# Optimization experiments

Hardware: AMD Instinct MI355X
Metric: run time of the kernel (lower is better)

## Reference

```python
import jax, jax.numpy as jnp
import numpy as np

BN_EPS = 1e-5


def setup_inputs() -> dict:
    key = jax.random.key(0)
    ks = jax.random.split(key, 12)
    B, C, N = 8, 256, 2048
    s = 1.0 / np.sqrt(C)
    x = jax.random.normal(ks[0], (B, C, N), dtype=jnp.float32)
    gamma = jnp.ones((C,), jnp.float32)
    beta = jnp.zeros((C,), jnp.float32)
    Wq = jax.random.normal(ks[1], (C, C), jnp.float32) * s
    bq = jnp.zeros((C,), jnp.float32)
    Wk = jax.random.normal(ks[2], (C, C), jnp.float32) * s
    bk = jnp.zeros((C,), jnp.float32)
    Wv = jax.random.normal(ks[3], (C, C), jnp.float32) * s
    bv = jnp.zeros((C,), jnp.float32)
    Wp = jax.random.normal(ks[4], (C, C), jnp.float32) * s
    bp = jnp.zeros((C,), jnp.float32)
    return {"x": x, "gamma": gamma, "beta": beta, "Wq": Wq, "bq": bq,
            "Wk": Wk, "bk": bk, "Wv": Wv, "bv": bv, "Wp": Wp, "bp": bp}


def reference(x, gamma, beta, Wq, bq, Wk, bk, Wv, bv, Wp, bp):
    B, C, N = x.shape
    # BatchNorm1d (training-mode batch stats): normalize per channel over (B, N)
    mean = jnp.mean(x, axis=(0, 2), keepdims=True)            # [1,C,1]
    var = jnp.mean(jnp.square(x - mean), axis=(0, 2), keepdims=True)
    h = (x - mean) * jax.lax.rsqrt(var + BN_EPS)
    h = h * gamma[None, :, None] + beta[None, :, None]
    # 1x1 Conv1d projections == per-position channel GEMMs
    q = jnp.einsum('oc,bcn->bno', Wq, h) + bq[None, None, :]  # [B,N,C]
    k = jnp.einsum('oc,bcn->bon', Wk, h) + bk[None, :, None]  # [B,C,N]
    v = jnp.einsum('oc,bcn->bno', Wv, h) + bv[None, None, :]  # [B,N,C]
    scale = jnp.asarray(C, x.dtype) ** -0.5
    w = jnp.einsum('bnc,bcm->bnm', q, k) * scale              # [B,N,N]
    w = jax.nn.softmax(w, axis=-1)
    h = jnp.einsum('bnm,bmc->bnc', w, v)                      # [B,N,C]
    out = jnp.einsum('oc,bnc->bon', Wp, h) + bp[None, :, None]  # [B,C,N]
    return x + out
```

## Files before the change

### kernel.cpp

```cpp
#include <hip/hip_runtime.h>
#include <hip/hip_fp16.h>

typedef _Float16 f16x8 __attribute__((ext_vector_type(8)));
typedef _Float16 f16x4 __attribute__((ext_vector_type(4)));
typedef float f32x4 __attribute__((ext_vector_type(4)));
typedef float f32x16 __attribute__((ext_vector_type(16)));

#define MFMA16(a, b, c) __builtin_amdgcn_mfma_f32_16x16x32_f16(a, b, c, 0, 0, 0)
#define MFMA32(a, b, c) __builtin_amdgcn_mfma_f32_32x32x16_f16(a, b, c, 0, 0, 0)

__device__ __forceinline__ void gload_lds16(const _Float16* g, void* l) {
    __builtin_amdgcn_global_load_lds(
        (const __attribute__((address_space(1))) void*)g,
        (__attribute__((address_space(3))) void*)l, 16, 0, 0);
}

__device__ __forceinline__ unsigned pkh(float a, float b) {
    typedef __fp16 fp16v2 __attribute__((ext_vector_type(2)));
    fp16v2 h = __builtin_amdgcn_cvt_pkrtz(a, b);
    return __builtin_bit_cast(unsigned, h);
}

__device__ __forceinline__ float fexp2(float x) {
#if __has_builtin(__builtin_amdgcn_exp2f)
    return __builtin_amdgcn_exp2f(x);
#else
    return exp2f(x);
#endif
}

__global__ __launch_bounds__(256) void trans_stats_kernel(
    const float* __restrict__ x, _Float16* __restrict__ xt,
    float* __restrict__ sums)
{
    __shared__ float tile[64][65];
    int t = threadIdx.x;
    int b = blockIdx.z, c0 = blockIdx.y * 64, n0 = blockIdx.x * 64;
    int nl = t & 63, cq = t >> 6;
#pragma unroll
    for (int r = 0; r < 16; ++r) {
        int cl = cq * 16 + r;
        tile[cl][nl] = x[((size_t)b * 256 + c0 + cl) * 2048 + n0 + nl];
    }
    __syncthreads();
    int cl2 = t & 63, nq = t >> 6;
#pragma unroll
    for (int r = 0; r < 16; ++r) {
        int nl2 = nq * 16 + r;
        xt[((size_t)b * 2048 + n0 + nl2) * 256 + c0 + cl2] = (_Float16)tile[cl2][nl2];
    }
    if (t < 64) {
        float s = 0.f, ss = 0.f;
#pragma unroll
        for (int j = 0; j < 64; ++j) {
            float v = tile[t][j];
            s += v; ss += v * v;
        }
        atomicAdd(&sums[c0 + t], s);
        atomicAdd(&sums[256 + c0 + t], ss);
    }
}

__global__ __launch_bounds__(256) void fold_kernel(
    const float* __restrict__ Wq, const float* __restrict__ Wk,
    const float* __restrict__ Wv, const float* __restrict__ Wp,
    const float* __restrict__ bq, const float* __restrict__ bk,
    const float* __restrict__ bv,
    const float* __restrict__ gamma, const float* __restrict__ beta,
    const float* __restrict__ sums,
    _Float16* __restrict__ wbf, float* __restrict__ bfold)
{
    int t = threadIdx.x, bid = blockIdx.x;
    if (bid >= 192) {
        int i = (bid - 192) * 256 + t;
        wbf[3 * 65536 + i] = (_Float16)Wp[i];
        return;
    }
    __shared__ float sc[256], sh[256];
    if (t < 256) {
        float mean = sums[t] * (1.f / 16384.f);
        float var  = sums[256 + t] * (1.f / 16384.f) - mean * mean;
        float rstd = rsqrtf(var + 1e-5f);
        float s = rstd * gamma[t];
        sc[t] = s;
        sh[t] = beta[t] - mean * s;
    }
    __syncthreads();
    const float QS = 0.09016844005556021f;
    int mat = bid >> 6;
    int o = (bid & 63) * 4 + (t >> 6);
    int lane = t & 63;
    const float* W  = (mat == 0) ? Wq : (mat == 1) ? Wk : Wv;
    const float* bb = (mat == 0) ? bq : (mat == 1) ? bk : bv;
    float qs = (mat == 0) ? QS : 1.f;
    float dot = 0.f;
    _Float16* wd = wbf + mat * 65536 + o * 256;
#pragma unroll
    for (int i = 0; i < 4; ++i) {
        int c = lane * 4 + i;
        float wv_ = W[o * 256 + c];
        dot += wv_ * sh[c];
        wd[c] = (_Float16)(wv_ * sc[c] * qs);
    }
#pragma unroll
    for (int off = 32; off > 0; off >>= 1) dot += __shfl_down(dot, off, 64);
    if (lane == 0) bfold[mat * 256 + o] = qs * (bb[o] + dot);
}

template<int BN, int WGM, int WGN, typename OT, bool BIAS_I, bool RES, int EPI>
__global__ __launch_bounds__(256, 3) void gemm_nt(
    const _Float16* __restrict__ Aall, long strideA,
    const _Float16* __restrict__ Ball, long strideB,
    const float* __restrict__ bias,
    const float* __restrict__ resid, long strideR,
    OT* __restrict__ Call, long strideC, int Nn)
{
    constexpr int BM = 128;
    constexpr int WR = BM / WGM;
    constexpr int WC = BN / WGN;
    constexpr int FM = WR / 16, FN = WC / 16;
    constexpr int BUFSZ = 8192 + BN * 64;
    constexpr int NI = 8 + BN / 16;
    constexpr int PW = NI / 4;

    int b = blockIdx.z;
    const _Float16* A  = Aall + (size_t)b * strideA;
    const _Float16* Bm = Ball + (size_t)b * strideB;
    OT* C = Call + (size_t)b * strideC;
    int i0 = blockIdx.y * BM, j0 = blockIdx.x * BN;

    __shared__ __align__(16) char lds[2 * BUFSZ];

    int t = threadIdx.x, lane = t & 63, w = t >> 6;
    int lr = lane & 15, lg = lane >> 4;
    int wm = w % WGM, wn = w / WGM;

    int soff = (lane >> 2) * 256 + (((lane & 3) ^ ((lane >> 3) & 3))) * 8;
    int lgx16 = ((lg ^ ((lr >> 1) & 3))) * 16;

    f32x4 acc[FM][FN] = {};

    auto stage = [&](int kk, int buf) {
#pragma unroll
        for (int i = 0; i < PW; ++i) {
            int u = w * PW + i;
            if (u < 8)
                gload_lds16(A + (size_t)(i0 + u * 16) * 256 + kk * 32 + soff,
                            lds + buf * BUFSZ + u * 1024);
            else
                gload_lds16(Bm + (size_t)(j0 + (u - 8) * 16) * 256 + kk * 32 + soff,
                            lds + buf * BUFSZ + 8192 + (u - 8) * 1024);
        }
    };

    stage(0, 0);
    __syncthreads();
    int buf = 0;
#pragma unroll
    for (int kk = 0; kk < 8; ++kk) {
        if (kk + 1 < 8) stage(kk + 1, buf ^ 1);
        const char* ab = lds + buf * BUFSZ;
        const char* bb = ab + 8192;
        f16x8 af[FM], bf[FN];
#pragma unroll
        for (int f = 0; f < FM; ++f)
            af[f] = *(const f16x8*)(ab + (wm * WR + f * 16 + lr) * 64 + lgx16);
#pragma unroll
        for (int f = 0; f < FN; ++f)
            bf[f] = *(const f16x8*)(bb + (wn * WC + f * 16 + lr) * 64 + lgx16);
        __builtin_amdgcn_s_setprio(1);
#pragma unroll
        for (int fm = 0; fm < FM; ++fm)
#pragma unroll
            for (int fn = 0; fn < FN; ++fn)
                acc[fm][fn] = MFMA16(af[fm], bf[fn], acc[fm][fn]);
        __builtin_amdgcn_s_setprio(0);
        __syncthreads();
        buf ^= 1;
    }
    if constexpr (EPI == 0) {
#pragma unroll
        for (int fm = 0; fm < FM; ++fm)
#pragma unroll
            for (int fn = 0; fn < FN; ++fn)
#pragma unroll
                for (int rr = 0; rr < 4; ++rr) {
                    int row = i0 + wm * WR + fm * 16 + lg * 4 + rr;
                    int col = j0 + wn * WC + fn * 16 + lr;
                    float vv = acc[fm][fn][rr] + (BIAS_I ? bias[row] : bias[col]);
                    if (RES) vv += resid[(size_t)b * strideR + (size_t)row * Nn + col];
                    C[(size_t)row * Nn + col] = (OT)vv;
                }
    } else {
#pragma unroll
        for (int fm = 0; fm < FM; ++fm)
#pragma unroll
            for (int fn = 0; fn < FN; ++fn) {
                int row0 = i0 + wm * WR + fm * 16 + lg * 4;
                int col  = j0 + wn * WC + fn * 16 + lr;
                f16x4 q4;
#pragma unroll
                for (int rr = 0; rr < 4; ++rr) {
                    float vv = acc[fm][fn][rr] + (BIAS_I ? bias[row0 + rr] : bias[col]);
                    q4[rr] = (_Float16)vv;
                }
                size_t off;
                if constexpr (EPI == 1) {
                    int mt = col >> 5, mloc = col & 31;
                    int ks = row0 >> 4;
                    int ln2 = mloc + 32 * (lg >> 1);
                    off = (((size_t)mt * 16 + ks) * 64 + ln2) * 8 + (lg & 1) * 4;
                } else {
                    int mt = row0 >> 5, ms = (row0 >> 4) & 1;
                    int dt = col >> 5, dloc = col & 31;
                    int ln2 = dloc + 32 * (lg >> 1);
                    off = ((((size_t)mt * 2 + ms) * 8 + dt) * 64 + ln2) * 8 + (lg & 1) * 4;
                }
                *(f16x4*)((_Float16*)C + off) = q4;
            }
    }
}

__global__ __launch_bounds__(256, 2) void attn8_kernel(
    const _Float16* __restrict__ qb, const _Float16* __restrict__ kfrag,
    const _Float16* __restrict__ vfrag,
    _Float16* __restrict__ Opart, float* __restrict__ lpart,
    int nsp, int mspan)
{
    int id = blockIdx.x;
    int b = id & 7;
    int rest = id >> 3;
    int qblk = rest & 15, sp = rest >> 4;
    int T = mspan >> 5;

    __shared__ __align__(16) char lds[66560];

    int t = threadIdx.x, ln = t & 63, w = t >> 6;
    int col = ln & 31, hi = ln >> 5;

    const _Float16* kg = kfrag + (size_t)b * 524288 + (size_t)(sp * T) * 8192 + ln * 8;
    const _Float16* vg = vfrag + (size_t)b * 524288 + (size_t)(sp * T) * 8192 + ln * 8;
    int c0 = w * 4;
    int frd = ln * 16;

    f16x8 qf[16];
    {
        const _Float16* qp = qb + ((size_t)b * 2048 + qblk * 128 + w * 32 + col) * 256 + hi * 8;
#pragma unroll
        for (int ks = 0; ks < 16; ++ks) qf[ks] = *(const f16x8*)(qp + ks * 16);
    }

    f32x16 oacc[8] = {};
    float l_run = 0.f;
    unsigned W[8];

#pragma unroll
    for (int i = 0; i < 4; ++i) {
        int c = c0 + i;
        gload_lds16(kg + c * 512,        lds + c * 1024);
        gload_lds16(vg + c * 512,        lds + 16384 + c * 1024);
        gload_lds16(kg + 8192 + c * 512, lds + 32768 + c * 1024);
        gload_lds16(vg + 8192 + c * 512, lds + 49152 + c * 1024);
    }
    asm volatile("s_waitcnt vmcnt(0)" ::: "memory");
    __builtin_amdgcn_sched_barrier(0);
    __builtin_amdgcn_s_barrier();
    {
        f32x16 sn = {};
        __builtin_amdgcn_s_setprio(1);
#pragma unroll
        for (int ks = 0; ks < 16; ++ks) {
            f16x8 kf = *(const f16x8*)(lds + ks * 1024 + frd);
            sn = MFMA32(kf, qf[ks], sn);
        }
        __builtin_amdgcn_s_setprio(0);
        float pv_[16];
#pragma unroll
        for (int i = 0; i < 16; ++i) pv_[i] = fexp2(sn[i] - 16.f);
        float psum = ((pv_[0]+pv_[1]) + (pv_[2]+pv_[3])) + ((pv_[4]+pv_[5]) + (pv_[6]+pv_[7]))
                   + ((pv_[8]+pv_[9]) + (pv_[10]+pv_[11])) + ((pv_[12]+pv_[13]) + (pv_[14]+pv_[15]));
        psum += __shfl_xor(psum, 32, 64);
        l_run = psum;
        W[0] = pkh(pv_[0],  pv_[1]);  W[1] = pkh(pv_[2],  pv_[3]);
        W[2] = pkh(pv_[4],  pv_[5]);  W[3] = pkh(pv_[6],  pv_[7]);
        W[4] = pkh(pv_[8],  pv_[9]);  W[5] = pkh(pv_[10], pv_[11]);
        W[6] = pkh(pv_[12], pv_[13]); W[7] = pkh(pv_[14], pv_[15]);
    }
    __builtin_amdgcn_s_barrier();

    for (int tt = 0; tt < T - 1; ++tt) {
        char* myb = lds + (tt & 1) * 32768;
        char* nxb = lds + ((tt + 1) & 1) * 32768;
        if (tt + 2 < T) {
            const _Float16* ks2 = kg + (size_t)(tt + 2) * 8192;
#pragma unroll
            for (int i = 0; i < 4; ++i)
                gload_lds16(ks2 + (c0 + i) * 512, myb + (c0 + i) * 1024);
        }
        union { unsigned u[4]; f16x8 v; } pf0, pf1;
        {
            unsigned sx0 = hi ? W[0] : W[2], sx1 = hi ? W[1] : W[3];
            unsigned r0 = __shfl_xor(sx0, 32, 64), r1 = __shfl_xor(sx1, 32, 64);
            pf0.u[0] = hi ? r0 : W[0]; pf0.u[1] = hi ? r1 : W[1];
            pf0.u[2] = hi ? W[2] : r0; pf0.u[3] = hi ? W[3] : r1;
        }
        {
            unsigned sx0 = hi ? W[4] : W[6], sx1 = hi ? W[5] : W[7];
            unsigned r0 = __shfl_xor(sx0, 32, 64), r1 = __shfl_xor(sx1, 32, 64);
            pf1.u[0] = hi ? r0 : W[4]; pf1.u[1] = hi ? r1 : W[5];
            pf1.u[2] = hi ? W[6] : r0; pf1.u[3] = hi ? W[7] : r1;
        }
        f32x16 sn = {};
        __builtin_amdgcn_s_setprio(1);
#pragma unroll
        for (int g = 0; g < 4; ++g) {
#pragma unroll
            for (int k2 = 0; k2 < 4; ++k2) {
                int ks = g * 4 + k2;
                f16x8 kf = *(const f16x8*)(nxb + ks * 1024 + frd);
                sn = MFMA32(kf, qf[ks], sn);
            }
#pragma unroll
            for (int k2 = 0; k2 < 4; ++k2) {
                int idx = g * 4 + k2;
                f16x8 vf = *(const f16x8*)(myb + 16384 + idx * 1024 + frd);
                oacc[idx & 7] = MFMA32(vf, (g < 2) ? pf0.v : pf1.v, oacc[idx & 7]);
            }
        }
        __builtin_amdgcn_s_setprio(0);
        {
            float pv_[16];
#pragma unroll
            for (int i = 0; i < 16; ++i) pv_[i] = fexp2(sn[i] - 16.f);
            float psum = ((pv_[0]+pv_[1]) + (pv_[2]+pv_[3])) + ((pv_[4]+pv_[5]) + (pv_[6]+pv_[7]))
                       + ((pv_[8]+pv_[9]) + (pv_[10]+pv_[11])) + ((pv_[12]+pv_[13]) + (pv_[14]+pv_[15]));
            psum += __shfl_xor(psum, 32, 64);
            l_run += psum;
            W[0] = pkh(pv_[0],  pv_[1]);  W[1] = pkh(pv_[2],  pv_[3]);
            W[2] = pkh(pv_[4],  pv_[5]);  W[3] = pkh(pv_[6],  pv_[7]);
            W[4] = pkh(pv_[8],  pv_[9]);  W[5] = pkh(pv_[10], pv_[11]);
            W[6] = pkh(pv_[12], pv_[13]); W[7] = pkh(pv_[14], pv_[15]);
        }
        __builtin_amdgcn_s_barrier();
        __builtin_amdgcn_sched_barrier(0);
        if (tt + 2 < T) {
            const _Float16* vs2 = vg + (size_t)(tt + 2) * 8192;
#pragma unroll
            for (int i = 0; i < 4; ++i)
                gload_lds16(vs2 + (c0 + i) * 512, myb + 16384 + (c0 + i) * 1024);
        }
        asm volatile("s_waitcnt vmcnt(4)" ::: "memory");
        __builtin_amdgcn_sched_barrier(0);
        __builtin_amdgcn_s_barrier();
    }

    asm volatile("s_waitcnt vmcnt(0)" ::: "memory");
    __builtin_amdgcn_sched_barrier(0);
    __builtin_amdgcn_s_barrier();
    {
        char* myb = lds + ((T - 1) & 1) * 32768;
        union { unsigned u[4]; f16x8 v; } pf0, pf1;
        {
            unsigned sx0 = hi ? W[0] : W[2], sx1 = hi ? W[1] : W[3];
            unsigned r0 = __shfl_xor(sx0, 32, 64), r1 = __shfl_xor(sx1, 32, 64);
            pf0.u[0] = hi ? r0 : W[0]; pf0.u[1] = hi ? r1 : W[1];
            pf0.u[2] = hi ? W[2] : r0; pf0.u[3] = hi ? W[3] : r1;
        }
        {
            unsigned sx0 = hi ? W[4] : W[6], sx1 = hi ? W[5] : W[7];
            unsigned r0 = __shfl_xor(sx0, 32, 64), r1 = __shfl_xor(sx1, 32, 64);
            pf1.u[0] = hi ? r0 : W[4]; pf1.u[1] = hi ? r1 : W[5];
            pf1.u[2] = hi ? W[6] : r0; pf1.u[3] = hi ? W[7] : r1;
        }
        __builtin_amdgcn_s_setprio(1);
#pragma unroll
        for (int idx = 0; idx < 16; ++idx) {
            f16x8 vf = *(const f16x8*)(myb + 16384 + idx * 1024 + frd);
            oacc[idx & 7] = MFMA32(vf, (idx < 8) ? pf0.v : pf1.v, oacc[idx & 7]);
        }
        __builtin_amdgcn_s_setprio(0);
    }
    __builtin_amdgcn_s_barrier();

    _Float16* tr = (_Float16*)(lds + w * 16640);
    float invl = 1.0f / l_run;
#pragma unroll
    for (int dt = 0; dt < 8; ++dt)
#pragma unroll
        for (int g = 0; g < 4; ++g) {
            f16x4 q4;
#pragma unroll
            for (int e = 0; e < 4; ++e) q4[e] = (_Float16)(oacc[dt][g * 4 + e] * invl);
            int d0 = dt * 32 + g * 8 + 4 * hi;
            *(f16x4*)(tr + col * 260 + d0) = q4;
        }
    size_t region = ((size_t)((sp * 8 + b) * 16 + qblk)) * 32768;
    int rrow = ln >> 1, h = ln & 1;
    const _Float16* srcr = tr + rrow * 260 + h * 128;
    _Float16* dstr = Opart + region + (size_t)(w * 32 + rrow) * 256 + h * 128;
#pragma unroll
    for (int i = 0; i < 16; ++i)
        *(f16x8*)(dstr + i * 8) = *(const f16x8*)(srcr + i * 8);

    if (hi == 0) {
        int qi = w * 32 + col;
        lpart[((sp * 8 + b) * 16 + qblk) * 128 + qi] = l_run;
    }
}

__global__ __launch_bounds__(256) void combine3_kernel(
    const _Float16* __restrict__ Opart, const float* __restrict__ lpart,
    _Float16* __restrict__ abuf, int nsp)
{
    int id = blockIdx.x;
    int b = id & 7, qb = (id >> 3) & 15, dh = id >> 7;
    int t = threadIdx.x;
    __shared__ float cf[4][128];
    if (t < 128) {
        float l[4], s = 0.f;
        for (int sp = 0; sp < nsp; ++sp) {
            l[sp] = lpart[((sp * 8 + b) * 16 + qb) * 128 + t];
            s += l[sp];
        }
        float inv = 1.0f / s;
        for (int sp = 0; sp < nsp; ++sp) cf[sp][t] = l[sp] * inv;
    }
    __syncthreads();
    size_t rb = ((size_t)(b * 16 + qb)) * 32768;
#pragma unroll
    for (int i = 0; i < 8; ++i) {
        int flat = i * 2048 + t * 8;
        int qi = flat >> 7, dl = flat & 127;
        float acc[8] = {};
        for (int sp = 0; sp < nsp; ++sp) {
            f16x8 v = *(const f16x8*)(Opart + (size_t)sp * 4194304 + rb +
                                      (size_t)qi * 256 + dh * 128 + dl);
            float c = cf[sp][qi];
#pragma unroll
            for (int e = 0; e < 8; ++e) acc[e] += c * (float)v[e];
        }
        f16x8 r;
#pragma unroll
        for (int e = 0; e < 8; ++e) r[e] = (_Float16)acc[e];
        *(f16x8*)(abuf + ((size_t)b * 2048 + qb * 128 + qi) * 256 + dh * 128 + dl) = r;
    }
}

extern "C" void kernel_launch(void* const* d_in, const int* in_sizes, int n_in,
                              void* d_out, int out_size, void* d_ws, size_t ws_size,
                              hipStream_t stream) {
    const float* x     = (const float*)d_in[0];
    const float* gamma = (const float*)d_in[1];
    const float* beta  = (const float*)d_in[2];
    const float* Wq    = (const float*)d_in[3];
    const float* bq    = (const float*)d_in[4];
    const float* Wk    = (const float*)d_in[5];
    const float* bk    = (const float*)d_in[6];
    const float* Wv    = (const float*)d_in[7];
    const float* bv    = (const float*)d_in[8];
    const float* Wp    = (const float*)d_in[9];
    const float* bp    = (const float*)d_in[10];
    float* out = (float*)d_out;

    char* ws = (char*)d_ws;
    float* sums  = (float*)ws;
    float* bfold = (float*)(ws + 2048);
    float* lpart = (float*)(ws + 8192);
    _Float16* wbf   = (_Float16*)(ws + 524288);
    _Float16* xt    = (_Float16*)(ws + 1048576);
    _Float16* qbuf  = (_Float16*)(ws + 9437184);
    _Float16* kfrag = (_Float16*)(ws + 17825792);
    _Float16* vfrag = (_Float16*)(ws + 26214400);
    _Float16* Opart = (_Float16*)(ws + 34603008);
    _Float16* abuf  = xt;

    int nsp = (ws_size >= (size_t)34603008 + 4ull * 8388608ull) ? 4 : 2;
    int mspan = 2048 / nsp;

    const long SB = 524288;

    hipMemsetAsync(sums, 0, 2048, stream);
    trans_stats_kernel<<<dim3(32, 4, 8), 256, 0, stream>>>(x, xt, sums);
    fold_kernel<<<448, 256, 0, stream>>>(Wq, Wk, Wv, Wp, bq, bk, bv,
                                         gamma, beta, sums, wbf, bfold);
    gemm_nt<64, 4, 1, _Float16, false, false, 0><<<dim3(4, 16, 8), 256, 0, stream>>>(
        xt, SB, wbf, 0, bfold, nullptr, 0, qbuf, SB, 256);
    gemm_nt<64, 4, 1, _Float16, true, false, 1><<<dim3(32, 2, 8), 256, 0, stream>>>(
        wbf + 65536, 0, xt, SB, bfold + 256, nullptr, 0, kfrag, SB, 2048);
    gemm_nt<64, 4, 1, _Float16, false, false, 2><<<dim3(4, 16, 8), 256, 0, stream>>>(
        xt, SB, wbf + 131072, 0, bfold + 512, nullptr, 0, vfrag, SB, 256);
    attn8_kernel<<<128 * nsp, 256, 0, stream>>>(qbuf, kfrag, vfrag, Opart, lpart,
                                                nsp, mspan);
    combine3_kernel<<<256, 256, 0, stream>>>(Opart, lpart, abuf, nsp);
    gemm_nt<64, 4, 1, float, true, true, 0><<<dim3(32, 2, 8), 256, 0, stream>>>(
        wbf + 196608, 0, abuf, SB, bp, x, SB, out, SB, 2048);
}
```

Measured before the change: 112.5 us.

## Triple-buffer V in attention and fuse Q/V projection GEMMs into one launch

The attention kernel now gives K two LDS slots and V three, so the prefetch of K and V for step tt+2 is issued together at the top of each iteration. This removes the mid-iteration barrier that used to gate the V prefetch, at the cost of more LDS per block (81920 bytes). Separately, the fold kernel lays out the Q and V weights next to each other, so one 128-wide-tile GEMM computes both Q and V and writes V in fragment layout to a second output. This saves a launch and a second read of xt.

```diff
diff --git a/kernel.cpp b/kernel.cpp
--- a/kernel.cpp
+++ b/kernel.cpp
@@ -93,8 +93,9 @@
     const float* W  = (mat == 0) ? Wq : (mat == 1) ? Wk : Wv;
     const float* bb = (mat == 0) ? bq : (mat == 1) ? bk : bv;
     float qs = (mat == 0) ? QS : 1.f;
+    int wslot = (mat == 0) ? 0 : (mat == 1) ? 131072 : 65536;
     float dot = 0.f;
-    _Float16* wd = wbf + mat * 65536 + o * 256;
+    _Float16* wd = wbf + wslot + o * 256;
 #pragma unroll
     for (int i = 0; i < 4; ++i) {
         int c = lane * 4 + i;
@@ -113,7 +114,8 @@
     const _Float16* __restrict__ Ball, long strideB,
     const float* __restrict__ bias,
     const float* __restrict__ resid, long strideR,
-    OT* __restrict__ Call, long strideC, int Nn)
+    OT* __restrict__ Call, long strideC, int Nn,
+    OT* __restrict__ Cauxall)
 {
     constexpr int BM = 128;
     constexpr int WR = BM / WGM;
@@ -191,7 +193,7 @@
                     if (RES) vv += resid[(size_t)b * strideR + (size_t)row * Nn + col];
                     C[(size_t)row * Nn + col] = (OT)vv;
                 }
-    } else {
+    } else if constexpr (EPI == 1) {
 #pragma unroll
         for (int fm = 0; fm < FM; ++fm)
 #pragma unroll
@@ -200,28 +202,47 @@
                 int col  = j0 + wn * WC + fn * 16 + lr;
                 f16x4 q4;
 #pragma unroll
-                for (int rr = 0; rr < 4; ++rr) {
-                    float vv = acc[fm][fn][rr] + (BIAS_I ? bias[row0 + rr] : bias[col]);
-                    q4[rr] = (_Float16)vv;
-                }
-                size_t off;
-                if constexpr (EPI == 1) {
-                    int mt = col >> 5, mloc = col & 31;
-                    int ks = row0 >> 4;
-                    int ln2 = mloc + 32 * (lg >> 1);
-                    off = (((size_t)mt * 16 + ks) * 64 + ln2) * 8 + (lg & 1) * 4;
-                } else {
-                    int mt = row0 >> 5, ms = (row0 >> 4) & 1;
-                    int dt = col >> 5, dloc = col & 31;
-                    int ln2 = dloc + 32 * (lg >> 1);
-                    off = ((((size_t)mt * 2 + ms) * 8 + dt) * 64 + ln2) * 8 + (lg & 1) * 4;
-                }
+                for (int rr = 0; rr < 4; ++rr)
+                    q4[rr] = (_Float16)(acc[fm][fn][rr] + bias[row0 + rr]);
+                int mt = col >> 5, mloc = col & 31;
+                int ks = row0 >> 4;
+                int ln2 = mloc + 32 * (lg >> 1);
+                size_t off = (((size_t)mt * 16 + ks) * 64 + ln2) * 8 + (lg & 1) * 4;
                 *(f16x4*)((_Float16*)C + off) = q4;
             }
-    }
-}
-
-__global__ __launch_bounds__(256, 2) void attn8_kernel(
+    } else {
+        bool vreg = (EPI == 2) || (j0 >= 256);
+#pragma unroll
+        for (int fm = 0; fm < FM; ++fm)
+#pragma unroll
+            for (int fn = 0; fn < FN; ++fn) {
+                int row0 = i0 + wm * WR + fm * 16 + lg * 4;
+                int col  = j0 + wn * WC + fn * 16 + lr;
+                if (vreg) {
+                    int colv = (EPI == 3) ? col - 256 : col;
+                    const float bv_ = (EPI == 3) ? bias[256 + col] : bias[colv];
+                    f16x4 q4;
+#pragma unroll
+                    for (int rr = 0; rr < 4; ++rr)
+                        q4[rr] = (_Float16)(acc[fm][fn][rr] + bv_);
+                    int mt = row0 >> 5, ms = (row0 >> 4) & 1;
+                    int dt = colv >> 5, dloc = colv & 31;
+                    int ln2 = dloc + 32 * (lg >> 1);
+                    size_t off = ((((size_t)mt * 2 + ms) * 8 + dt) * 64 + ln2) * 8 + (lg & 1) * 4;
+                    OT* dst = (EPI == 3) ? (Cauxall + (size_t)b * strideC) : C;
+                    *(f16x4*)((_Float16*)dst + off) = q4;
+                } else {
+#pragma unroll
+                    for (int rr = 0; rr < 4; ++rr) {
+                        float vv = acc[fm][fn][rr] + bias[col];
+                        C[(size_t)(row0 + rr) * 256 + col] = (OT)vv;
+                    }
+                }
+            }
+    }
+}
+
+__global__ __launch_bounds__(256, 2) void attn9_kernel(
     const _Float16* __restrict__ qb, const _Float16* __restrict__ kfrag,
     const _Float16* __restrict__ vfrag,
     _Float16* __restrict__ Opart, float* __restrict__ lpart,
@@ -233,7 +254,7 @@
     int qblk = rest & 15, sp = rest >> 4;
     int T = mspan >> 5;
 
-    __shared__ __align__(16) char lds[66560];
+    __shared__ __align__(16) char lds[81920];
 
     int t = threadIdx.x, ln = t & 63, w = t >> 6;
     int col = ln & 31, hi = ln >> 5;
@@ -258,8 +279,8 @@
     for (int i = 0; i < 4; ++i) {
         int c = c0 + i;
         gload_lds16(kg + c * 512,        lds + c * 1024);
-        gload_lds16(vg + c * 512,        lds + 16384 + c * 1024);
-        gload_lds16(kg + 8192 + c * 512, lds + 32768 + c * 1024);
+        gload_lds16(kg + 8192 + c * 512, lds + 16384 + c * 1024);
+        gload_lds16(vg + c * 512,        lds + 32768 + c * 1024);
         gload_lds16(vg + 8192 + c * 512, lds + 49152 + c * 1024);
     }
     asm volatile("s_waitcnt vmcnt(0)" ::: "memory");
@@ -289,13 +310,18 @@
     __builtin_amdgcn_s_barrier();
 
     for (int tt = 0; tt < T - 1; ++tt) {
-        char* myb = lds + (tt & 1) * 32768;
-        char* nxb = lds + ((tt + 1) & 1) * 32768;
+        const char* kb = lds + ((tt + 1) & 1) * 16384;
+        const char* vb = lds + 32768 + (tt % 3) * 16384;
         if (tt + 2 < T) {
-            const _Float16* ks2 = kg + (size_t)(tt + 2) * 8192;
-#pragma unroll
-            for (int i = 0; i < 4; ++i)
-                gload_lds16(ks2 + (c0 + i) * 512, myb + (c0 + i) * 1024);
+            const _Float16* sK = kg + (size_t)(tt + 2) * 8192;
+            const _Float16* sV = vg + (size_t)(tt + 2) * 8192;
+            char* kd = lds + (tt & 1) * 16384;
+            char* vd = lds + 32768 + ((tt + 2) % 3) * 16384;
+#pragma unroll
+            for (int i = 0; i < 4; ++i) {
+                gload_lds16(sK + (c0 + i) * 512, kd + (c0 + i) * 1024);
+                gload_lds16(sV + (c0 + i) * 512, vd + (c0 + i) * 1024);
+            }
         }
         union { unsigned u[4]; f16x8 v; } pf0, pf1;
         {
@@ -317,13 +343,13 @@
 #pragma unroll
             for (int k2 = 0; k2 < 4; ++k2) {
                 int ks = g * 4 + k2;
-                f16x8 kf = *(const f16x8*)(nxb + ks * 1024 + frd);
+                f16x8 kf = *(const f16x8*)(kb + ks * 1024 + frd);
                 sn = MFMA32(kf, qf[ks], sn);
             }
 #pragma unroll
             for (int k2 = 0; k2 < 4; ++k2) {
                 int idx = g * 4 + k2;
-                f16x8 vf = *(const f16x8*)(myb + 16384 + idx * 1024 + frd);
+                f16x8 vf = *(const f16x8*)(vb + 16384 * 0 + idx * 1024 + frd);
                 oacc[idx & 7] = MFMA32(vf, (g < 2) ? pf0.v : pf1.v, oacc[idx & 7]);
             }
         }
@@ -341,14 +367,6 @@
             W[4] = pkh(pv_[8],  pv_[9]);  W[5] = pkh(pv_[10], pv_[11]);
             W[6] = pkh(pv_[12], pv_[13]); W[7] = pkh(pv_[14], pv_[15]);
         }
-        __builtin_amdgcn_s_barrier();
-        __builtin_amdgcn_sched_barrier(0);
-        if (tt + 2 < T) {
-            const _Float16* vs2 = vg + (size_t)(tt + 2) * 8192;
-#pragma unroll
-            for (int i = 0; i < 4; ++i)
-                gload_lds16(vs2 + (c0 + i) * 512, myb + 16384 + (c0 + i) * 1024);
-        }
         asm volatile("s_waitcnt vmcnt(4)" ::: "memory");
         __builtin_amdgcn_sched_barrier(0);
         __builtin_amdgcn_s_barrier();
@@ -358,7 +376,7 @@
     __builtin_amdgcn_sched_barrier(0);
     __builtin_amdgcn_s_barrier();
     {
-        char* myb = lds + ((T - 1) & 1) * 32768;
+        const char* vb = lds + 32768 + ((T - 1) % 3) * 16384;
         union { unsigned u[4]; f16x8 v; } pf0, pf1;
         {
             unsigned sx0 = hi ? W[0] : W[2], sx1 = hi ? W[1] : W[3];
@@ -375,7 +393,7 @@
         __builtin_amdgcn_s_setprio(1);
 #pragma unroll
         for (int idx = 0; idx < 16; ++idx) {
-            f16x8 vf = *(const f16x8*)(myb + 16384 + idx * 1024 + frd);
+            f16x8 vf = *(const f16x8*)(vb + idx * 1024 + frd);
             oacc[idx & 7] = MFMA32(vf, (idx < 8) ? pf0.v : pf1.v, oacc[idx & 7]);
         }
         __builtin_amdgcn_s_setprio(0);
@@ -483,15 +501,13 @@
     trans_stats_kernel<<<dim3(32, 4, 8), 256, 0, stream>>>(x, xt, sums);
     fold_kernel<<<448, 256, 0, stream>>>(Wq, Wk, Wv, Wp, bq, bk, bv,
                                          gamma, beta, sums, wbf, bfold);
-    gemm_nt<64, 4, 1, _Float16, false, false, 0><<<dim3(4, 16, 8), 256, 0, stream>>>(
-        xt, SB, wbf, 0, bfold, nullptr, 0, qbuf, SB, 256);
+    gemm_nt<128, 2, 2, _Float16, false, false, 3><<<dim3(4, 16, 8), 256, 0, stream>>>(
+        xt, SB, wbf, 0, bfold, nullptr, 0, qbuf, SB, 256, vfrag);
     gemm_nt<64, 4, 1, _Float16, true, false, 1><<<dim3(32, 2, 8), 256, 0, stream>>>(
-        wbf + 65536, 0, xt, SB, bfold + 256, nullptr, 0, kfrag, SB, 2048);
-    gemm_nt<64, 4, 1, _Float16, false, false, 2><<<dim3(4, 16, 8), 256, 0, stream>>>(
-        xt, SB, wbf + 131072, 0, bfold + 512, nullptr, 0, vfrag, SB, 256);
-    attn8_kernel<<<128 * nsp, 256, 0, stream>>>(qbuf, kfrag, vfrag, Opart, lpart,
+        wbf + 131072, 0, xt, SB, bfold + 256, nullptr, 0, kfrag, SB, 2048, (_Float16*)nullptr);
+    attn9_kernel<<<128 * nsp, 256, 0, stream>>>(qbuf, kfrag, vfrag, Opart, lpart,
                                                 nsp, mspan);
     combine3_kernel<<<256, 256, 0, stream>>>(Opart, lpart, abuf, nsp);
     gemm_nt<64, 4, 1, float, true, true, 0><<<dim3(32, 2, 8), 256, 0, stream>>>(
-        wbf + 196608, 0, abuf, SB, bp, x, SB, out, SB, 2048);
-}
+        wbf + 196608, 0, abuf, SB, bp, x, SB, out, SB, 2048, (float*)nullptr);
+}
```

After: 108.2 us. -3.8%, faster.
